# Kernel tuning notes

Hardware: AMD Instinct MI355X
Metric: run time of the kernel (lower is better)

## Reference

```python
import jax, jax.numpy as jnp
import numpy as np

N_HEAD = 16
N_EMBD = 1024
HEAD_DIM = N_EMBD // N_HEAD


def setup_inputs() -> dict:
    key = jax.random.key(0)
    k1, k2, k3 = jax.random.split(key, 3)
    B, T, C = 2, 2048, N_EMBD
    x = jax.random.normal(k1, (B, T, C), dtype=jnp.float32)
    # nn.Linear weights: (out_features, in_features)
    W_attn = jax.random.normal(k2, (3 * C, C), dtype=jnp.float32) * 0.02
    W_proj = jax.random.normal(k3, (C, C), dtype=jnp.float32) * 0.02
    return {"x": x, "W_attn": W_attn, "W_proj": W_proj}


def reference(x, W_attn, W_proj):
    B, T, C = x.shape
    h, hd = N_HEAD, HEAD_DIM
    # c_attn: x @ W^T, then split into q, k, v
    qkv = jnp.einsum('btc,dc->btd', x, W_attn)  # [B, T, 3C]
    q, k, v = jnp.split(qkv, 3, axis=-1)
    # [B, T, C] -> [B, h, T, hd]
    q = q.reshape(B, T, h, hd).transpose(0, 2, 1, 3)
    k = k.reshape(B, T, h, hd).transpose(0, 2, 1, 3)
    v = v.reshape(B, T, h, hd).transpose(0, 2, 1, 3)
    # NOTE: no 1/sqrt(hd) scaling in the original module
    logits = jnp.einsum('bhnk,bhmk->bhnm', q, k)  # [B, h, T, T]
    causal = jnp.tril(jnp.ones((T, T), dtype=bool))  # [T, T]
    logits = jnp.where(causal[None, None, :, :], logits, -jnp.inf)
    weights = jax.nn.softmax(logits, axis=-1)
    O = jnp.einsum('bhnm,bhmv->bhnv', weights, v)  # [B, h, T, hd]
    # Original: einsum('bhnv,hdv->bnd', O, c_proj.weight) with weight viewed as (h, d, v)
    Wp = W_proj.reshape(h, C, hd)
    Y = jnp.einsum('bhnv,hdv->bnd', O, Wp)  # [B, T, C]
    return Y
```

## Files before the change

### kernel.cpp

```cpp
#include <hip/hip_runtime.h>
#include <stdint.h>
#include <math.h>

#define B_    2
#define T_    2048
#define C_    1024
#define H_    16
#define D_    64
#define MTOT  4096
#define NQKV  3072
#define KDIM  1024

typedef short short8 __attribute__((ext_vector_type(8)));
typedef float f32x4  __attribute__((ext_vector_type(4)));

__device__ __forceinline__ uint16_t f2b(float f) {
    union { float f; uint32_t u; } x; x.f = f;
    uint32_t u = x.u;
    return (uint16_t)((u + 0x7FFFu + ((u >> 16) & 1u)) >> 16);
}
__device__ __forceinline__ uint32_t packb2(float a, float b) {
    union { float f; uint32_t u; } x, y; x.f = a; y.f = b;
    return ((x.u + 0x8000u) >> 16) | ((y.u + 0x8000u) & 0xffff0000u);
}
__device__ __forceinline__ uint32_t packb2_rne(float a, float b) {
    return (uint32_t)f2b(a) | ((uint32_t)f2b(b) << 16);
}

__device__ __forceinline__ void gload_lds16(const uint16_t* g, uint16_t* l) {
    __builtin_amdgcn_global_load_lds((const __attribute__((address_space(1))) void*)g,
                                     (__attribute__((address_space(3))) void*)l, 16, 0, 0);
}

__global__ __launch_bounds__(256) void cast_f32_bf16(const float* __restrict__ in,
                                                     uint16_t* __restrict__ out, int n4) {
    int i = blockIdx.x * blockDim.x + threadIdx.x;
    if (i < n4) {
        float4 v = ((const float4*)in)[i];
        ushort4 o;
        o.x = f2b(v.x); o.y = f2b(v.y); o.z = f2b(v.z); o.w = f2b(v.w);
        ((ushort4*)out)[i] = o;
    }
}

__global__ __launch_bounds__(256) void cast_wp(const float* __restrict__ wp,
                                               uint16_t* __restrict__ wt) {
    int i = blockIdx.x * blockDim.x + threadIdx.x;
    int j4 = (i & 255) * 4;
    int d  = i >> 8;
    int h = j4 >> 6, v = j4 & 63;
    float4 val = *(const float4*)(wp + h * 65536 + d * 64 + v);
    ushort4 o;
    o.x = f2b(val.x); o.y = f2b(val.y); o.z = f2b(val.z); o.w = f2b(val.w);
    *(ushort4*)(wt + d * 1024 + j4) = o;
}

__global__ __launch_bounds__(256) void gemm_qkv(const uint16_t* __restrict__ A,
                                                const uint16_t* __restrict__ Bw,
                                                uint16_t* __restrict__ qkvb) {
    __shared__ __align__(16) uint16_t As[128 * 64];
    __shared__ __align__(16) uint16_t Bs[128 * 64];

    int tid = threadIdx.x;
    int w = tid >> 6, lane = tid & 63;
    int qd = lane >> 4, ln = lane & 15;
    int lnx = ln & 7;
    int rowBase = blockIdx.y * 128;
    int colBase = blockIdx.x * 128;
    int mw = (w >> 1) * 64, nw = (w & 1) * 64;

    int srow = tid >> 3;
    int pchunk = tid & 7;
    int gchunk = pchunk ^ (srow & 7);

    f32x4 acc[4][4] = {};
    for (int k0 = 0; k0 < KDIM; k0 += 64) {
        const uint16_t* ga = A  + (size_t)(rowBase + srow) * KDIM + k0 + gchunk * 8;
        const uint16_t* gb = Bw + (size_t)(colBase + srow) * KDIM + k0 + gchunk * 8;
        uint16_t* la = &As[srow * 64 + pchunk * 8];
        uint16_t* lb = &Bs[srow * 64 + pchunk * 8];
#pragma unroll
        for (int m = 0; m < 4; m++) {
            gload_lds16(ga + (size_t)m * 32 * KDIM, la + m * 32 * 64);
            gload_lds16(gb + (size_t)m * 32 * KDIM, lb + m * 32 * 64);
        }
        __syncthreads();

        short8 a[4][2], b[4][2];
#pragma unroll
        for (int i = 0; i < 4; i++)
#pragma unroll
            for (int ks = 0; ks < 2; ks++) {
                int p = (ks * 4 + qd) ^ lnx;
                a[i][ks] = *(const short8*)&As[(mw + i * 16 + ln) * 64 + p * 8];
                b[i][ks] = *(const short8*)&Bs[(nw + i * 16 + ln) * 64 + p * 8];
            }
#pragma unroll
        for (int ks = 0; ks < 2; ks++)
#pragma unroll
            for (int i = 0; i < 4; i++)
#pragma unroll
                for (int j = 0; j < 4; j++)
                    acc[i][j] = __builtin_amdgcn_mfma_f32_16x16x32_bf16(a[i][ks], b[j][ks], acc[i][j], 0, 0, 0);
        __syncthreads();
    }

#pragma unroll
    for (int i = 0; i < 4; i++) {
#pragma unroll
        for (int j = 0; j < 4; j++) {
            int gcol = colBase + nw + j * 16 + ln;
            int which = gcol >> 10;
            int rem = gcol & 1023;
            int h = rem >> 6, d = rem & 63;
#pragma unroll
            for (int r = 0; r < 4; r++) {
                int grow = rowBase + mw + i * 16 + qd * 4 + r;
                int bb = grow >> 11, t = grow & 2047;
                uint16_t val = f2b(acc[i][j][r]);
                if (which == 2) {
                    qkvb[(size_t)2 * 4194304 + (((size_t)(bb * H_ + h) * D_) + d) * T_ + t] = val;
                } else {
                    qkvb[(size_t)which * 4194304 + (((size_t)(bb * H_ + h) * T_) + t) * D_ + d] = val;
                }
            }
        }
    }
}

__global__ __launch_bounds__(128) void attn(const uint16_t* __restrict__ qkvb,
                                            uint16_t* __restrict__ oc) {
    union ShU {
        uint16_t Pl[2][64][72];
        struct { f32x4 Cb[16][64]; float Lb[64][4]; } c;
    };
    __shared__ __align__(16) ShU sh;

    int tid = threadIdx.x;
    int w = tid >> 6, lane = tid & 63;
    int qd = lane >> 4, ln = lane & 15;
    int bid = blockIdx.x;
    int qt = 31 - (bid >> 5);
    int bh = bid & 31;
    int qbase = qt * 64;
    int ntiles = qt + 1;

    const uint16_t* Q  = qkvb + (size_t)bh * T_ * D_;
    const uint16_t* K  = Q + 4194304;
    const uint16_t* Vt = qkvb + (size_t)2 * 4194304 + (size_t)bh * D_ * T_;

    short8 bq[4][2];
#pragma unroll
    for (int jq = 0; jq < 4; jq++)
#pragma unroll
        for (int ks = 0; ks < 2; ks++)
            bq[jq][ks] = *(const short8*)(Q + (size_t)(qbase + jq * 16 + ln) * D_ + ks * 32 + qd * 8);

    f32x4 ot[4][4] = {};
    float l_part[4] = {};

    for (int kt = w; kt < ntiles; kt += 2) {
        short8 ak[4][2], av[4][2];
#pragma unroll
        for (int it = 0; it < 4; it++)
#pragma unroll
            for (int ks = 0; ks < 2; ks++)
                ak[it][ks] = *(const short8*)(K + (size_t)(kt * 64 + it * 16 + ln) * D_ + ks * 32 + qd * 8);
#pragma unroll
        for (int id = 0; id < 4; id++)
#pragma unroll
            for (int ks = 0; ks < 2; ks++)
                av[id][ks] = *(const short8*)(Vt + (size_t)(id * 16 + ln) * T_ + kt * 64 + ks * 32 + qd * 8);

        f32x4 st[4][4] = {};
#pragma unroll
        for (int ks = 0; ks < 2; ks++)
#pragma unroll
            for (int it = 0; it < 4; it++)
#pragma unroll
                for (int jq = 0; jq < 4; jq++)
                    st[it][jq] = __builtin_amdgcn_mfma_f32_16x16x32_bf16(ak[it][ks], bq[jq][ks], st[it][jq], 0, 0, 0);

        if (kt == qt) {
#pragma unroll
            for (int it = 0; it < 4; it++)
#pragma unroll
                for (int jq = 0; jq < 4; jq++)
#pragma unroll
                    for (int r = 0; r < 4; r++) {
                        int t = it * 16 + qd * 4 + r;
                        int q = jq * 16 + ln;
                        if (t > q) st[it][jq][r] = -1.0e30f;
                    }
        }

#pragma unroll
        for (int it = 0; it < 4; it++)
#pragma unroll
            for (int jq = 0; jq < 4; jq++) {
                float p0 = __expf(st[it][jq][0]);
                float p1 = __expf(st[it][jq][1]);
                float p2 = __expf(st[it][jq][2]);
                float p3 = __expf(st[it][jq][3]);
                l_part[jq] += (p0 + p1) + (p2 + p3);
                uint2 pk;
                pk.x = packb2(p0, p1);
                pk.y = packb2(p2, p3);
                *(uint2*)&sh.Pl[w][jq * 16 + ln][it * 16 + qd * 4] = pk;
            }

        short8 bp[4][2];
#pragma unroll
        for (int jq = 0; jq < 4; jq++)
#pragma unroll
            for (int ks = 0; ks < 2; ks++)
                bp[jq][ks] = *(const short8*)&sh.Pl[w][jq * 16 + ln][ks * 32 + qd * 8];

#pragma unroll
        for (int ks = 0; ks < 2; ks++)
#pragma unroll
            for (int id = 0; id < 4; id++)
#pragma unroll
                for (int jq = 0; jq < 4; jq++)
                    ot[id][jq] = __builtin_amdgcn_mfma_f32_16x16x32_bf16(av[id][ks], bp[jq][ks], ot[id][jq], 0, 0, 0);
    }

    __syncthreads();
    if (w == 1) {
#pragma unroll
        for (int id = 0; id < 4; id++)
#pragma unroll
            for (int jq = 0; jq < 4; jq++)
                sh.c.Cb[id * 4 + jq][lane] = ot[id][jq];
        f32x4 lp = { l_part[0], l_part[1], l_part[2], l_part[3] };
        *(f32x4*)&sh.c.Lb[lane][0] = lp;
    }
    __syncthreads();
    if (w == 0) {
#pragma unroll
        for (int id = 0; id < 4; id++)
#pragma unroll
            for (int jq = 0; jq < 4; jq++)
                ot[id][jq] += sh.c.Cb[id * 4 + jq][lane];
        f32x4 lo = *(const f32x4*)&sh.c.Lb[lane][0];
        float rl[4];
#pragma unroll
        for (int jq = 0; jq < 4; jq++) {
            float s = l_part[jq] + lo[jq];
            s += __shfl_xor(s, 16);
            s += __shfl_xor(s, 32);
            rl[jq] = 1.0f / s;
        }
        int b = bh >> 4, h = bh & 15;
#pragma unroll
        for (int id = 0; id < 4; id++)
#pragma unroll
            for (int jq = 0; jq < 4; jq++) {
                float v0 = ot[id][jq][0] * rl[jq];
                float v1 = ot[id][jq][1] * rl[jq];
                float v2 = ot[id][jq][2] * rl[jq];
                float v3 = ot[id][jq][3] * rl[jq];
                uint2 pk;
                pk.x = packb2_rne(v0, v1);
                pk.y = packb2_rne(v2, v3);
                int q = qbase + jq * 16 + ln;
                *(uint2*)&oc[(size_t)(b * T_ + q) * C_ + h * 64 + id * 16 + qd * 4] = pk;
            }
    }
}

__global__ __launch_bounds__(256) void gemm_out(const uint16_t* __restrict__ A,
                                                const uint16_t* __restrict__ Bw,
                                                float* __restrict__ out) {
    __shared__ __align__(16) uint16_t As[128 * 64];
    __shared__ __align__(16) uint16_t Bs[64 * 64];

    int tid = threadIdx.x;
    int w = tid >> 6, lane = tid & 63;
    int qd = lane >> 4, ln = lane & 15;
    int lnx = ln & 7;
    int rowBase = blockIdx.y * 128;
    int colBase = blockIdx.x * 64;
    int mw = (w >> 1) * 64, nw = (w & 1) * 32;

    int srow = tid >> 3;
    int pchunk = tid & 7;
    int gchunk = pchunk ^ (srow & 7);

    f32x4 acc[4][2] = {};
    for (int k0 = 0; k0 < KDIM; k0 += 64) {
        const uint16_t* ga = A  + (size_t)(rowBase + srow) * KDIM + k0 + gchunk * 8;
        const uint16_t* gb = Bw + (size_t)(colBase + srow) * KDIM + k0 + gchunk * 8;
        uint16_t* la = &As[srow * 64 + pchunk * 8];
        uint16_t* lb = &Bs[srow * 64 + pchunk * 8];
#pragma unroll
        for (int m = 0; m < 4; m++)
            gload_lds16(ga + (size_t)m * 32 * KDIM, la + m * 32 * 64);
#pragma unroll
        for (int m = 0; m < 2; m++)
            gload_lds16(gb + (size_t)m * 32 * KDIM, lb + m * 32 * 64);
        __syncthreads();

        short8 a[4][2], b[2][2];
#pragma unroll
        for (int ks = 0; ks < 2; ks++) {
            int p = (ks * 4 + qd) ^ lnx;
#pragma unroll
            for (int i = 0; i < 4; i++)
                a[i][ks] = *(const short8*)&As[(mw + i * 16 + ln) * 64 + p * 8];
#pragma unroll
            for (int j = 0; j < 2; j++)
                b[j][ks] = *(const short8*)&Bs[(nw + j * 16 + ln) * 64 + p * 8];
        }
#pragma unroll
        for (int ks = 0; ks < 2; ks++)
#pragma unroll
            for (int i = 0; i < 4; i++)
#pragma unroll
                for (int j = 0; j < 2; j++)
                    acc[i][j] = __builtin_amdgcn_mfma_f32_16x16x32_bf16(a[i][ks], b[j][ks], acc[i][j], 0, 0, 0);
        __syncthreads();
    }

#pragma unroll
    for (int i = 0; i < 4; i++)
#pragma unroll
        for (int j = 0; j < 2; j++)
#pragma unroll
            for (int r = 0; r < 4; r++) {
                int grow = rowBase + mw + i * 16 + qd * 4 + r;
                int gcol = colBase + nw + j * 16 + ln;
                out[(size_t)grow * 1024 + gcol] = acc[i][j][r];
            }
}

extern "C" void kernel_launch(void* const* d_in, const int* in_sizes, int n_in,
                              void* d_out, int out_size, void* d_ws, size_t ws_size,
                              hipStream_t stream) {
    const float* x  = (const float*)d_in[0];
    const float* Wa = (const float*)d_in[1];
    const float* Wp = (const float*)d_in[2];
    float* out = (float*)d_out;

    uint16_t* ws   = (uint16_t*)d_ws;
    uint16_t* xb   = ws;
    uint16_t* Wab  = xb + 4194304;
    uint16_t* Wtb  = Wab + 3145728;
    uint16_t* qkvb = Wtb + 1048576;
    uint16_t* ob   = qkvb + (size_t)3 * 4194304;

    cast_f32_bf16<<<4096, 256, 0, stream>>>(x, xb, 4194304 / 4);
    cast_f32_bf16<<<3072, 256, 0, stream>>>(Wa, Wab, 3145728 / 4);
    cast_wp<<<1024, 256, 0, stream>>>(Wp, Wtb);
    gemm_qkv<<<dim3(24, 32), 256, 0, stream>>>(xb, Wab, qkvb);
    attn<<<1024, 128, 0, stream>>>(qkvb, ob);
    gemm_out<<<dim3(16, 32), 256, 0, stream>>>(ob, Wtb, out);
}
```

Baseline: 192.6 us.

## Register-prefetch GEMM tiles, fold log2e into Q, fuse cast kernels

Both GEMMs replace direct global-to-LDS loads with register prefetch of the next K tile, overlapping global loads with MFMA work, and add an occupancy hint of 3 blocks per CU. Q is pre-scaled by log2(e) in the QKV epilogue so attention can use the hardware exp2 instead of expf, and the score computation is restructured per row tile to lower register pressure. The two f32-to-bf16 cast launches are merged into one. The costs are extra registers for the prefetch buffers and possible spilling under the tighter launch bound. Rounding Q after the scale also shifts bf16 rounding slightly.

```diff
diff --git a/kernel.cpp b/kernel.cpp
--- a/kernel.cpp
+++ b/kernel.cpp
@@ -11,6 +11,8 @@
 #define NQKV  3072
 #define KDIM  1024
 
+#define LOG2E 1.4426950408889634f
+
 typedef short short8 __attribute__((ext_vector_type(8)));
 typedef float f32x4  __attribute__((ext_vector_type(4)));
 
@@ -26,21 +28,27 @@
 __device__ __forceinline__ uint32_t packb2_rne(float a, float b) {
     return (uint32_t)f2b(a) | ((uint32_t)f2b(b) << 16);
 }
-
-__device__ __forceinline__ void gload_lds16(const uint16_t* g, uint16_t* l) {
-    __builtin_amdgcn_global_load_lds((const __attribute__((address_space(1))) void*)g,
-                                     (__attribute__((address_space(3))) void*)l, 16, 0, 0);
-}
-
-__global__ __launch_bounds__(256) void cast_f32_bf16(const float* __restrict__ in,
-                                                     uint16_t* __restrict__ out, int n4) {
+__device__ __forceinline__ float fexp2(float x) {
+#if __has_builtin(__builtin_amdgcn_exp2f)
+    return __builtin_amdgcn_exp2f(x);
+#else
+    return exp2f(x);
+#endif
+}
+
+__global__ __launch_bounds__(256) void cast_all(const float* __restrict__ x,
+                                                const float* __restrict__ wa,
+                                                uint16_t* __restrict__ xb,
+                                                uint16_t* __restrict__ wab,
+                                                int n4x, int n4w) {
     int i = blockIdx.x * blockDim.x + threadIdx.x;
-    if (i < n4) {
-        float4 v = ((const float4*)in)[i];
-        ushort4 o;
-        o.x = f2b(v.x); o.y = f2b(v.y); o.z = f2b(v.z); o.w = f2b(v.w);
-        ((ushort4*)out)[i] = o;
-    }
+    const float* src; uint16_t* dst; int j;
+    if (i < n4x) { src = x; dst = xb; j = i; }
+    else { j = i - n4x; if (j >= n4w) return; src = wa; dst = wab; }
+    float4 v = ((const float4*)src)[j];
+    ushort4 o;
+    o.x = f2b(v.x); o.y = f2b(v.y); o.z = f2b(v.z); o.w = f2b(v.w);
+    ((ushort4*)dst)[j] = o;
 }
 
 __global__ __launch_bounds__(256) void cast_wp(const float* __restrict__ wp,
@@ -55,9 +63,9 @@
     *(ushort4*)(wt + d * 1024 + j4) = o;
 }
 
-__global__ __launch_bounds__(256) void gemm_qkv(const uint16_t* __restrict__ A,
-                                                const uint16_t* __restrict__ Bw,
-                                                uint16_t* __restrict__ qkvb) {
+__global__ __launch_bounds__(256, 3) void gemm_qkv(const uint16_t* __restrict__ A,
+                                                   const uint16_t* __restrict__ Bw,
+                                                   uint16_t* __restrict__ qkvb) {
     __shared__ __align__(16) uint16_t As[128 * 64];
     __shared__ __align__(16) uint16_t Bs[128 * 64];
 
@@ -73,35 +81,49 @@
     int pchunk = tid & 7;
     int gchunk = pchunk ^ (srow & 7);
 
+    const uint16_t* ga = A  + (size_t)(rowBase + srow) * KDIM + gchunk * 8;
+    const uint16_t* gb = Bw + (size_t)(colBase + srow) * KDIM + gchunk * 8;
+    uint16_t* la = &As[srow * 64 + pchunk * 8];
+    uint16_t* lb = &Bs[srow * 64 + pchunk * 8];
+
+    short8 pa[4], pb[4];
+#pragma unroll
+    for (int m = 0; m < 4; m++) {
+        pa[m] = *(const short8*)(ga + (size_t)m * 32 * KDIM);
+        pb[m] = *(const short8*)(gb + (size_t)m * 32 * KDIM);
+    }
+
     f32x4 acc[4][4] = {};
-    for (int k0 = 0; k0 < KDIM; k0 += 64) {
-        const uint16_t* ga = A  + (size_t)(rowBase + srow) * KDIM + k0 + gchunk * 8;
-        const uint16_t* gb = Bw + (size_t)(colBase + srow) * KDIM + k0 + gchunk * 8;
-        uint16_t* la = &As[srow * 64 + pchunk * 8];
-        uint16_t* lb = &Bs[srow * 64 + pchunk * 8];
+    for (int s = 0; s < 16; s++) {
 #pragma unroll
         for (int m = 0; m < 4; m++) {
-            gload_lds16(ga + (size_t)m * 32 * KDIM, la + m * 32 * 64);
-            gload_lds16(gb + (size_t)m * 32 * KDIM, lb + m * 32 * 64);
+            *(short8*)(la + m * 32 * 64) = pa[m];
+            *(short8*)(lb + m * 32 * 64) = pb[m];
         }
         __syncthreads();
-
-        short8 a[4][2], b[4][2];
-#pragma unroll
-        for (int i = 0; i < 4; i++)
-#pragma unroll
-            for (int ks = 0; ks < 2; ks++) {
-                int p = (ks * 4 + qd) ^ lnx;
-                a[i][ks] = *(const short8*)&As[(mw + i * 16 + ln) * 64 + p * 8];
-                b[i][ks] = *(const short8*)&Bs[(nw + i * 16 + ln) * 64 + p * 8];
-            }
-#pragma unroll
-        for (int ks = 0; ks < 2; ks++)
+        if (s < 15) {
+            int k0 = (s + 1) * 64;
+#pragma unroll
+            for (int m = 0; m < 4; m++) {
+                pa[m] = *(const short8*)(ga + k0 + (size_t)m * 32 * KDIM);
+                pb[m] = *(const short8*)(gb + k0 + (size_t)m * 32 * KDIM);
+            }
+        }
+#pragma unroll
+        for (int ks = 0; ks < 2; ks++) {
+            int p = (ks * 4 + qd) ^ lnx;
+            short8 a[4], b[4];
+#pragma unroll
+            for (int i = 0; i < 4; i++) {
+                a[i] = *(const short8*)&As[(mw + i * 16 + ln) * 64 + p * 8];
+                b[i] = *(const short8*)&Bs[(nw + i * 16 + ln) * 64 + p * 8];
+            }
 #pragma unroll
             for (int i = 0; i < 4; i++)
 #pragma unroll
                 for (int j = 0; j < 4; j++)
-                    acc[i][j] = __builtin_amdgcn_mfma_f32_16x16x32_bf16(a[i][ks], b[j][ks], acc[i][j], 0, 0, 0);
+                    acc[i][j] = __builtin_amdgcn_mfma_f32_16x16x32_bf16(a[i], b[j], acc[i][j], 0, 0, 0);
+        }
         __syncthreads();
     }
 
@@ -113,11 +135,12 @@
             int which = gcol >> 10;
             int rem = gcol & 1023;
             int h = rem >> 6, d = rem & 63;
+            float sc = (which == 0) ? LOG2E : 1.0f;
 #pragma unroll
             for (int r = 0; r < 4; r++) {
                 int grow = rowBase + mw + i * 16 + qd * 4 + r;
                 int bb = grow >> 11, t = grow & 2047;
-                uint16_t val = f2b(acc[i][j][r]);
+                uint16_t val = f2b(acc[i][j][r] * sc);
                 if (which == 2) {
                     qkvb[(size_t)2 * 4194304 + (((size_t)(bb * H_ + h) * D_) + d) * T_ + t] = val;
                 } else {
@@ -172,42 +195,38 @@
             for (int ks = 0; ks < 2; ks++)
                 av[id][ks] = *(const short8*)(Vt + (size_t)(id * 16 + ln) * T_ + kt * 64 + ks * 32 + qd * 8);
 
-        f32x4 st[4][4] = {};
-#pragma unroll
-        for (int ks = 0; ks < 2; ks++)
-#pragma unroll
-            for (int it = 0; it < 4; it++)
+        bool diag = (kt == qt);
+#pragma unroll
+        for (int it = 0; it < 4; it++) {
+            f32x4 stt[4] = {};
+#pragma unroll
+            for (int ks = 0; ks < 2; ks++)
 #pragma unroll
                 for (int jq = 0; jq < 4; jq++)
-                    st[it][jq] = __builtin_amdgcn_mfma_f32_16x16x32_bf16(ak[it][ks], bq[jq][ks], st[it][jq], 0, 0, 0);
-
-        if (kt == qt) {
-#pragma unroll
-            for (int it = 0; it < 4; it++)
+                    stt[jq] = __builtin_amdgcn_mfma_f32_16x16x32_bf16(ak[it][ks], bq[jq][ks], stt[jq], 0, 0, 0);
+            if (diag) {
 #pragma unroll
                 for (int jq = 0; jq < 4; jq++)
 #pragma unroll
                     for (int r = 0; r < 4; r++) {
                         int t = it * 16 + qd * 4 + r;
                         int q = jq * 16 + ln;
-                        if (t > q) st[it][jq][r] = -1.0e30f;
+                        if (t > q) stt[jq][r] = -1.0e30f;
                     }
-        }
-
-#pragma unroll
-        for (int it = 0; it < 4; it++)
+            }
 #pragma unroll
             for (int jq = 0; jq < 4; jq++) {
-                float p0 = __expf(st[it][jq][0]);
-                float p1 = __expf(st[it][jq][1]);
-                float p2 = __expf(st[it][jq][2]);
-                float p3 = __expf(st[it][jq][3]);
+                float p0 = fexp2(stt[jq][0]);
+                float p1 = fexp2(stt[jq][1]);
+                float p2 = fexp2(stt[jq][2]);
+                float p3 = fexp2(stt[jq][3]);
                 l_part[jq] += (p0 + p1) + (p2 + p3);
                 uint2 pk;
                 pk.x = packb2(p0, p1);
                 pk.y = packb2(p2, p3);
                 *(uint2*)&sh.Pl[w][jq * 16 + ln][it * 16 + qd * 4] = pk;
             }
+        }
 
         short8 bp[4][2];
 #pragma unroll
@@ -269,9 +288,9 @@
     }
 }
 
-__global__ __launch_bounds__(256) void gemm_out(const uint16_t* __restrict__ A,
-                                                const uint16_t* __restrict__ Bw,
-                                                float* __restrict__ out) {
+__global__ __launch_bounds__(256, 3) void gemm_out(const uint16_t* __restrict__ A,
+                                                   const uint16_t* __restrict__ Bw,
+                                                   float* __restrict__ out) {
     __shared__ __align__(16) uint16_t As[128 * 64];
     __shared__ __align__(16) uint16_t Bs[64 * 64];
 
@@ -287,38 +306,53 @@
     int pchunk = tid & 7;
     int gchunk = pchunk ^ (srow & 7);
 
+    const uint16_t* ga = A  + (size_t)(rowBase + srow) * KDIM + gchunk * 8;
+    const uint16_t* gb = Bw + (size_t)(colBase + srow) * KDIM + gchunk * 8;
+    uint16_t* la = &As[srow * 64 + pchunk * 8];
+    uint16_t* lb = &Bs[srow * 64 + pchunk * 8];
+
+    short8 pa[4], pb[2];
+#pragma unroll
+    for (int m = 0; m < 4; m++)
+        pa[m] = *(const short8*)(ga + (size_t)m * 32 * KDIM);
+#pragma unroll
+    for (int m = 0; m < 2; m++)
+        pb[m] = *(const short8*)(gb + (size_t)m * 32 * KDIM);
+
     f32x4 acc[4][2] = {};
-    for (int k0 = 0; k0 < KDIM; k0 += 64) {
-        const uint16_t* ga = A  + (size_t)(rowBase + srow) * KDIM + k0 + gchunk * 8;
-        const uint16_t* gb = Bw + (size_t)(colBase + srow) * KDIM + k0 + gchunk * 8;
-        uint16_t* la = &As[srow * 64 + pchunk * 8];
-        uint16_t* lb = &Bs[srow * 64 + pchunk * 8];
+    for (int s = 0; s < 16; s++) {
 #pragma unroll
         for (int m = 0; m < 4; m++)
-            gload_lds16(ga + (size_t)m * 32 * KDIM, la + m * 32 * 64);
+            *(short8*)(la + m * 32 * 64) = pa[m];
 #pragma unroll
         for (int m = 0; m < 2; m++)
-            gload_lds16(gb + (size_t)m * 32 * KDIM, lb + m * 32 * 64);
+            *(short8*)(lb + m * 32 * 64) = pb[m];
         __syncthreads();
-
-        short8 a[4][2], b[2][2];
+        if (s < 15) {
+            int k0 = (s + 1) * 64;
+#pragma unroll
+            for (int m = 0; m < 4; m++)
+                pa[m] = *(const short8*)(ga + k0 + (size_t)m * 32 * KDIM);
+#pragma unroll
+            for (int m = 0; m < 2; m++)
+                pb[m] = *(const short8*)(gb + k0 + (size_t)m * 32 * KDIM);
+        }
 #pragma unroll
         for (int ks = 0; ks < 2; ks++) {
             int p = (ks * 4 + qd) ^ lnx;
+            short8 a[4], b[2];
 #pragma unroll
             for (int i = 0; i < 4; i++)
-                a[i][ks] = *(const short8*)&As[(mw + i * 16 + ln) * 64 + p * 8];
+                a[i] = *(const short8*)&As[(mw + i * 16 + ln) * 64 + p * 8];
 #pragma unroll
             for (int j = 0; j < 2; j++)
-                b[j][ks] = *(const short8*)&Bs[(nw + j * 16 + ln) * 64 + p * 8];
-        }
-#pragma unroll
-        for (int ks = 0; ks < 2; ks++)
+                b[j] = *(const short8*)&Bs[(nw + j * 16 + ln) * 64 + p * 8];
 #pragma unroll
             for (int i = 0; i < 4; i++)
 #pragma unroll
                 for (int j = 0; j < 2; j++)
-                    acc[i][j] = __builtin_amdgcn_mfma_f32_16x16x32_bf16(a[i][ks], b[j][ks], acc[i][j], 0, 0, 0);
+                    acc[i][j] = __builtin_amdgcn_mfma_f32_16x16x32_bf16(a[i], b[j], acc[i][j], 0, 0, 0);
+        }
         __syncthreads();
     }
 
@@ -349,8 +383,7 @@
     uint16_t* qkvb = Wtb + 1048576;
     uint16_t* ob   = qkvb + (size_t)3 * 4194304;
 
-    cast_f32_bf16<<<4096, 256, 0, stream>>>(x, xb, 4194304 / 4);
-    cast_f32_bf16<<<3072, 256, 0, stream>>>(Wa, Wab, 3145728 / 4);
+    cast_all<<<7168, 256, 0, stream>>>(x, Wa, xb, Wab, 4194304 / 4, 3145728 / 4);
     cast_wp<<<1024, 256, 0, stream>>>(Wp, Wtb);
     gemm_qkv<<<dim3(24, 32), 256, 0, stream>>>(xb, Wab, qkvb);
     attn<<<1024, 128, 0, stream>>>(qkvb, ob);
```

Result: faster. 174.9 us (-9.2%).
